# Kernel optimization log

Hardware: AMD Instinct MI355X
Metric: run time of the kernel (lower is better)

The kernel has to match this reference:

```python
import jax, jax.numpy as jnp
import numpy as np

IOU_THRESHOLD = 0.5
LOW_BG_IOU = 0.1      # below this -> ignored
IMG_SIZE = 1024.0


def _make_boxes(key, n):
    kxy, kwh = jax.random.split(key)
    xy = jax.random.uniform(kxy, (n, 2), dtype=jnp.float32, maxval=IMG_SIZE * 0.8)
    wh = jax.random.uniform(kwh, (n, 2), dtype=jnp.float32, minval=8.0, maxval=IMG_SIZE * 0.2)
    return jnp.concatenate([xy, xy + wh], axis=-1)  # valid x1<x2, y1<y2


def setup_inputs() -> dict:
    key = jax.random.key(0)
    k1, k2, k3 = jax.random.split(key, 3)
    proposals = _make_boxes(k1, 200000)          # [N,4]
    gt_boxes = _make_boxes(k2, 128)              # [G,4]
    gt_labels = jax.random.randint(k3, (128,), 1, 21, dtype=jnp.int64)  # [G]
    return {"proposals": proposals, "gt_boxes": gt_boxes, "gt_labels": gt_labels}


def get_iou(boxes1, boxes2):
    # boxes1: [G,4], boxes2: [N,4] -> iou [G,N]
    area1 = (boxes1[:, 2] - boxes1[:, 0]) * (boxes1[:, 3] - boxes1[:, 1])  # [G]
    area2 = (boxes2[:, 2] - boxes2[:, 0]) * (boxes2[:, 3] - boxes2[:, 1])  # [N]
    x1 = jnp.maximum(boxes1[:, None, 0], boxes2[None, :, 0])
    y1 = jnp.maximum(boxes1[:, None, 1], boxes2[None, :, 1])
    x2 = jnp.minimum(boxes1[:, None, 2], boxes2[None, :, 2])
    y2 = jnp.minimum(boxes1[:, None, 3], boxes2[None, :, 3])
    inter = jnp.clip(x2 - x1, 0.0) * jnp.clip(y2 - y1, 0.0)  # [G,N]
    union = area1[:, None] + area2[None, :] - inter
    return inter / union


def reference(proposals, gt_boxes, gt_labels):
    iou = get_iou(gt_boxes, proposals)                # [G,N]
    best_match_iou = jnp.max(iou, axis=0)             # [N]
    best_match_gt_idx = jnp.argmax(iou, axis=0)       # [N], >= 0
    background = (best_match_iou < IOU_THRESHOLD) & (best_match_iou >= LOW_BG_IOU)
    ignored = best_match_iou < LOW_BG_IOU
    # torch clamps the (-1/-2) sentinel indices back to 0 before the gather,
    # so gathering with the raw argmax index is identical.
    matched_gt_boxes = gt_boxes[best_match_gt_idx]    # [N,4]
    labels = gt_labels[best_match_gt_idx].astype(jnp.int64)
    labels = jnp.where(background, jnp.int64(0), labels)
    labels = jnp.where(ignored, jnp.int64(-1), labels)
    return labels, matched_gt_boxes
```

## Files before the change

### kernel.cpp

```cpp
#include <hip/hip_runtime.h>


#define BLOCK 256
#define IOU_THRESHOLD 0.5f
#define LOW_BG_IOU 0.1f

__global__ void pack_gt_kernel(const float* __restrict__ gt_boxes,
                               const int*   __restrict__ gt_labels,
                               float* __restrict__ rec, int G)
{
    int g = threadIdx.x + blockIdx.x * blockDim.x;
    if (g < G) {
        float4 b = ((const float4*)gt_boxes)[g];
        float* r = rec + g * 8;
        r[0] = b.x; r[1] = b.y; r[2] = b.z; r[3] = b.w;
        r[4] = (b.z - b.x) * (b.w - b.y);
        r[5] = (float)gt_labels[g];
        r[6] = 0.0f; r[7] = 0.0f;
    }
}

__global__ __launch_bounds__(BLOCK) void roi_match_kernel(
    const float* __restrict__ proposals,
    const float* __restrict__ rec,
    const float* __restrict__ gt_boxes,
    float* __restrict__ out,
    int N)
{
#pragma clang fp contract(off)
    int n = blockIdx.x * blockDim.x + threadIdx.x;
    if (n >= N) return;

    float4 p = ((const float4*)proposals)[n];
    float area_p = (p.z - p.x) * (p.w - p.y);

    int   bi = 0;
    float inter_b = 0.0f, uni_b = 1.0f;

#pragma unroll 8
    for (int g = 0; g < 128; ++g) {
        const float* r = rec + g * 8;
        float gx1 = r[0], gy1 = r[1], gx2 = r[2], gy2 = r[3], garea = r[4];

        float x1 = fmaxf(gx1, p.x);
        float y1 = fmaxf(gy1, p.y);
        float x2 = fminf(gx2, p.z);
        float y2 = fminf(gy2, p.w);
        float iw = fmaxf(x2 - x1, 0.0f);
        float ih = fmaxf(y2 - y1, 0.0f);
        float inter = iw * ih;
        float uni   = (garea + area_p) - inter;

        float p1 = inter * uni_b;
        float e1 = fmaf(inter, uni_b, -p1);
        float p2 = inter_b * uni;
        float e2 = fmaf(inter_b, uni, -p2);
        bool gt = (p1 - p2) > (e2 - e1);

        bi      = gt ? g     : bi;
        inter_b = gt ? inter : inter_b;
        uni_b   = gt ? uni   : uni_b;
    }

    float best = inter_b / uni_b;

    float lab;
    if (best < LOW_BG_IOU)          lab = -1.0f;
    else if (best < IOU_THRESHOLD)  lab = 0.0f;
    else                            lab = rec[bi * 8 + 5];

    out[n] = lab;
    ((float4*)(out + N))[n] = ((const float4*)gt_boxes)[bi];
}

extern "C" void kernel_launch(void* const* d_in, const int* in_sizes, int n_in,
                              void* d_out, int out_size, void* d_ws, size_t ws_size,
                              hipStream_t stream) {
    const float* proposals = (const float*)d_in[0];
    const float* gt_boxes  = (const float*)d_in[1];
    const int*   gt_labels = (const int*)d_in[2];
    float* out = (float*)d_out;
    float* rec = (float*)d_ws;

    int N = in_sizes[0] / 4;
    int G = in_sizes[1] / 4;

    pack_gt_kernel<<<1, 128, 0, stream>>>(gt_boxes, gt_labels, rec, G);

    int blocks = (N + BLOCK - 1) / BLOCK;
    roi_match_kernel<<<blocks, BLOCK, 0, stream>>>(proposals, rec, gt_boxes,
                                                   out, N);
}
```

Measured before the change: 86.05 us.

## Split GT loop across four waves per block with shared-memory reduction

Removes the separate GT packing kernel and instead has each block pack the 128 GT records into LDS. Each block now handles 64 proposals, with four waves each scanning 32 GTs. Partial best matches are combined in shared memory by wave 0, which keeps the exact tie-breaking comparison. This cuts the serial loop length per thread and the extra launch. The cost is 4x more blocks, each repeating the GT packing, plus a barrier and reduction step, with only one wave active for the final writes.

```diff
diff --git a/kernel.cpp b/kernel.cpp
--- a/kernel.cpp
+++ b/kernel.cpp
@@ -2,50 +2,56 @@
 
 
 #define BLOCK 256
+#define NPROP 64
+#define GT_TOTAL 128
+#define GT_PER_WAVE 32
 #define IOU_THRESHOLD 0.5f
 #define LOW_BG_IOU 0.1f
 
-__global__ void pack_gt_kernel(const float* __restrict__ gt_boxes,
-                               const int*   __restrict__ gt_labels,
-                               float* __restrict__ rec, int G)
-{
-    int g = threadIdx.x + blockIdx.x * blockDim.x;
-    if (g < G) {
-        float4 b = ((const float4*)gt_boxes)[g];
-        float* r = rec + g * 8;
-        r[0] = b.x; r[1] = b.y; r[2] = b.z; r[3] = b.w;
-        r[4] = (b.z - b.x) * (b.w - b.y);
-        r[5] = (float)gt_labels[g];
-        r[6] = 0.0f; r[7] = 0.0f;
-    }
-}
-
 __global__ __launch_bounds__(BLOCK) void roi_match_kernel(
     const float* __restrict__ proposals,
-    const float* __restrict__ rec,
     const float* __restrict__ gt_boxes,
+    const int*   __restrict__ gt_labels,
     float* __restrict__ out,
     int N)
 {
 #pragma clang fp contract(off)
-    int n = blockIdx.x * blockDim.x + threadIdx.x;
-    if (n >= N) return;
+    __shared__ float  s_rec[GT_TOTAL][8];
+    __shared__ float4 s_part[4][NPROP];
 
-    float4 p = ((const float4*)proposals)[n];
+    int tid = threadIdx.x;
+    if (tid < GT_TOTAL) {
+        float4 b = ((const float4*)gt_boxes)[tid];
+        s_rec[tid][0] = b.x; s_rec[tid][1] = b.y;
+        s_rec[tid][2] = b.z; s_rec[tid][3] = b.w;
+        s_rec[tid][4] = (b.z - b.x) * (b.w - b.y);
+        s_rec[tid][5] = (float)gt_labels[tid];
+        s_rec[tid][6] = 0.0f; s_rec[tid][7] = 0.0f;
+    }
+    __syncthreads();
+
+    int wave = tid >> 6;
+    int lane = tid & 63;
+    int n  = blockIdx.x * NPROP + lane;
+    int nc = n < N ? n : N - 1;
+
+    float4 p = ((const float4*)proposals)[nc];
     float area_p = (p.z - p.x) * (p.w - p.y);
 
-    int   bi = 0;
+    int g0 = wave * GT_PER_WAVE;
+    int   bi = g0;
     float inter_b = 0.0f, uni_b = 1.0f;
 
-#pragma unroll 8
-    for (int g = 0; g < 128; ++g) {
-        const float* r = rec + g * 8;
-        float gx1 = r[0], gy1 = r[1], gx2 = r[2], gy2 = r[3], garea = r[4];
+#pragma unroll 4
+    for (int j = 0; j < GT_PER_WAVE; ++j) {
+        int g = g0 + j;
+        float4 gb   = *(const float4*)&s_rec[g][0];
+        float garea = s_rec[g][4];
 
-        float x1 = fmaxf(gx1, p.x);
-        float y1 = fmaxf(gy1, p.y);
-        float x2 = fminf(gx2, p.z);
-        float y2 = fminf(gy2, p.w);
+        float x1 = fmaxf(gb.x, p.x);
+        float y1 = fmaxf(gb.y, p.y);
+        float x2 = fminf(gb.z, p.z);
+        float y2 = fminf(gb.w, p.w);
         float iw = fmaxf(x2 - x1, 0.0f);
         float ih = fmaxf(y2 - y1, 0.0f);
         float inter = iw * ih;
@@ -62,15 +68,37 @@
         uni_b   = gt ? uni   : uni_b;
     }
 
-    float best = inter_b / uni_b;
+    s_part[wave][lane] = make_float4(inter_b, uni_b, __int_as_float(bi), 0.0f);
+    __syncthreads();
 
-    float lab;
-    if (best < LOW_BG_IOU)          lab = -1.0f;
-    else if (best < IOU_THRESHOLD)  lab = 0.0f;
-    else                            lab = rec[bi * 8 + 5];
+    if (wave == 0 && n < N) {
+        float4 b0 = s_part[0][lane];
+        float binter = b0.x, buni = b0.y;
+        int   bbi = __float_as_int(b0.z);
+#pragma unroll
+        for (int w = 1; w < 4; ++w) {
+            float4 c = s_part[w][lane];
+            float ci = c.x, cu = c.y;
+            float p1 = ci * buni;
+            float e1 = fmaf(ci, buni, -p1);
+            float p2 = binter * cu;
+            float e2 = fmaf(binter, cu, -p2);
+            bool gt = (p1 - p2) > (e2 - e1);
+            bbi    = gt ? __float_as_int(c.z) : bbi;
+            binter = gt ? ci : binter;
+            buni   = gt ? cu : buni;
+        }
 
-    out[n] = lab;
-    ((float4*)(out + N))[n] = ((const float4*)gt_boxes)[bi];
+        float best = binter / buni;
+
+        float lab;
+        if (best < LOW_BG_IOU)          lab = -1.0f;
+        else if (best < IOU_THRESHOLD)  lab = 0.0f;
+        else                            lab = s_rec[bbi][5];
+
+        out[n] = lab;
+        ((float4*)(out + N))[n] = *(const float4*)&s_rec[bbi][0];
+    }
 }
 
 extern "C" void kernel_launch(void* const* d_in, const int* in_sizes, int n_in,
@@ -80,14 +108,10 @@
     const float* gt_boxes  = (const float*)d_in[1];
     const int*   gt_labels = (const int*)d_in[2];
     float* out = (float*)d_out;
-    float* rec = (float*)d_ws;
 
     int N = in_sizes[0] / 4;
-    int G = in_sizes[1] / 4;
+    int blocks = (N + NPROP - 1) / NPROP;
 
-    pack_gt_kernel<<<1, 128, 0, stream>>>(gt_boxes, gt_labels, rec, G);
-
-    int blocks = (N + BLOCK - 1) / BLOCK;
-    roi_match_kernel<<<blocks, BLOCK, 0, stream>>>(proposals, rec, gt_boxes,
-                                                   out, N);
+    roi_match_kernel<<<blocks, BLOCK, 0, stream>>>(proposals, gt_boxes,
+                                                   gt_labels, out, N);
 }
```

Result: faster. 72.88 us (-15.3%).

## Split GT loop across 16 waves per 64 proposals with shared-memory argmax reduction

Applied to the files above, without the earlier changes.

Each block now handles 64 proposals with 16 waves, each wave scanning 8 GT boxes held in registers, then reduces the per-wave best matches through two shared-memory stages using the same exact-comparison tie logic. The separate GT packing kernel is removed and labels and areas are computed inline, which drops one launch. This raises parallelism for a compute-bound loop, at the cost of redundant proposal loads per wave, barrier overhead and more blocks.

```diff
diff --git a/kernel.cpp b/kernel.cpp
--- a/kernel.cpp
+++ b/kernel.cpp
@@ -1,55 +1,54 @@
 #include <hip/hip_runtime.h>
 
 
-#define BLOCK 256
 #define IOU_THRESHOLD 0.5f
 #define LOW_BG_IOU 0.1f
 
-__global__ void pack_gt_kernel(const float* __restrict__ gt_boxes,
-                               const int*   __restrict__ gt_labels,
-                               float* __restrict__ rec, int G)
-{
-    int g = threadIdx.x + blockIdx.x * blockDim.x;
-    if (g < G) {
-        float4 b = ((const float4*)gt_boxes)[g];
-        float* r = rec + g * 8;
-        r[0] = b.x; r[1] = b.y; r[2] = b.z; r[3] = b.w;
-        r[4] = (b.z - b.x) * (b.w - b.y);
-        r[5] = (float)gt_labels[g];
-        r[6] = 0.0f; r[7] = 0.0f;
-    }
-}
-
-__global__ __launch_bounds__(BLOCK) void roi_match_kernel(
+__global__ __launch_bounds__(1024) void roi_match_kernel(
     const float* __restrict__ proposals,
-    const float* __restrict__ rec,
     const float* __restrict__ gt_boxes,
+    const int*   __restrict__ gt_labels,
     float* __restrict__ out,
     int N)
 {
 #pragma clang fp contract(off)
-    int n = blockIdx.x * blockDim.x + threadIdx.x;
-    if (n >= N) return;
+    __shared__ float4 s_a[16][64];
+    __shared__ float4 s_b[8][64];
 
-    float4 p = ((const float4*)proposals)[n];
-    float area_p = (p.z - p.x) * (p.w - p.y);
+    const int tid  = threadIdx.x;
+    const int wave = __builtin_amdgcn_readfirstlane(tid >> 6);
+    const int lane = tid & 63;
 
-    int   bi = 0;
+    const int n  = blockIdx.x * 64 + lane;
+    const int nc = n < N ? n : N - 1;
+
+    const float4 p = ((const float4*)proposals)[nc];
+    const float area_p = (p.z - p.x) * (p.w - p.y);
+
+    const int g0 = wave * 8;
+
+    float4 gb[8];
+    float  ga[8];
+#pragma unroll
+    for (int j = 0; j < 8; ++j)
+        gb[j] = ((const float4*)gt_boxes)[g0 + j];
+#pragma unroll
+    for (int j = 0; j < 8; ++j)
+        ga[j] = (gb[j].z - gb[j].x) * (gb[j].w - gb[j].y);
+
+    int   bi = g0;
     float inter_b = 0.0f, uni_b = 1.0f;
 
-#pragma unroll 8
-    for (int g = 0; g < 128; ++g) {
-        const float* r = rec + g * 8;
-        float gx1 = r[0], gy1 = r[1], gx2 = r[2], gy2 = r[3], garea = r[4];
-
-        float x1 = fmaxf(gx1, p.x);
-        float y1 = fmaxf(gy1, p.y);
-        float x2 = fminf(gx2, p.z);
-        float y2 = fminf(gy2, p.w);
+#pragma unroll
+    for (int j = 0; j < 8; ++j) {
+        float x1 = fmaxf(gb[j].x, p.x);
+        float y1 = fmaxf(gb[j].y, p.y);
+        float x2 = fminf(gb[j].z, p.z);
+        float y2 = fminf(gb[j].w, p.w);
         float iw = fmaxf(x2 - x1, 0.0f);
         float ih = fmaxf(y2 - y1, 0.0f);
         float inter = iw * ih;
-        float uni   = (garea + area_p) - inter;
+        float uni   = (ga[j] + area_p) - inter;
 
         float p1 = inter * uni_b;
         float e1 = fmaf(inter, uni_b, -p1);
@@ -57,20 +56,49 @@
         float e2 = fmaf(inter_b, uni, -p2);
         bool gt = (p1 - p2) > (e2 - e1);
 
-        bi      = gt ? g     : bi;
-        inter_b = gt ? inter : inter_b;
-        uni_b   = gt ? uni   : uni_b;
+        bi      = gt ? g0 + j : bi;
+        inter_b = gt ? inter  : inter_b;
+        uni_b   = gt ? uni    : uni_b;
     }
 
-    float best = inter_b / uni_b;
+    s_a[wave][lane] = make_float4(inter_b, uni_b, __int_as_float(bi), 0.0f);
+    __syncthreads();
 
-    float lab;
-    if (best < LOW_BG_IOU)          lab = -1.0f;
-    else if (best < IOU_THRESHOLD)  lab = 0.0f;
-    else                            lab = rec[bi * 8 + 5];
+    if (wave < 8) {
+        float4 a = s_a[2 * wave][lane];
+        float4 b = s_a[2 * wave + 1][lane];
+        float p1 = b.x * a.y;
+        float e1 = fmaf(b.x, a.y, -p1);
+        float p2 = a.x * b.y;
+        float e2 = fmaf(a.x, b.y, -p2);
+        bool gt = (p1 - p2) > (e2 - e1);
+        s_b[wave][lane] = gt ? b : a;
+    }
+    __syncthreads();
 
-    out[n] = lab;
-    ((float4*)(out + N))[n] = ((const float4*)gt_boxes)[bi];
+    if (wave == 0 && n < N) {
+        float4 best = s_b[0][lane];
+#pragma unroll
+        for (int w = 1; w < 8; ++w) {
+            float4 c = s_b[w][lane];
+            float p1 = c.x * best.y;
+            float e1 = fmaf(c.x, best.y, -p1);
+            float p2 = best.x * c.y;
+            float e2 = fmaf(best.x, c.y, -p2);
+            bool gt = (p1 - p2) > (e2 - e1);
+            best = gt ? c : best;
+        }
+        int bbi = __float_as_int(best.z);
+        float q = best.x / best.y;
+
+        float lab;
+        if (q < LOW_BG_IOU)          lab = -1.0f;
+        else if (q < IOU_THRESHOLD)  lab = 0.0f;
+        else                         lab = (float)gt_labels[bbi];
+
+        out[n] = lab;
+        ((float4*)(out + N))[n] = ((const float4*)gt_boxes)[bbi];
+    }
 }
 
 extern "C" void kernel_launch(void* const* d_in, const int* in_sizes, int n_in,
@@ -80,14 +108,10 @@
     const float* gt_boxes  = (const float*)d_in[1];
     const int*   gt_labels = (const int*)d_in[2];
     float* out = (float*)d_out;
-    float* rec = (float*)d_ws;
 
     int N = in_sizes[0] / 4;
-    int G = in_sizes[1] / 4;
+    int blocks = (N + 63) / 64;
 
-    pack_gt_kernel<<<1, 128, 0, stream>>>(gt_boxes, gt_labels, rec, G);
-
-    int blocks = (N + BLOCK - 1) / BLOCK;
-    roi_match_kernel<<<blocks, BLOCK, 0, stream>>>(proposals, rec, gt_boxes,
-                                                   out, N);
+    roi_match_kernel<<<blocks, 1024, 0, stream>>>(proposals, gt_boxes,
+                                                  gt_labels, out, N);
 }
```

Result: slower. 99.73 us (+15.9%).
